# Optimization experiments

Measured on AMD Instinct MI355X. Metric: run time of the kernel, lower is better.

## Reference

```python
import jax, jax.numpy as jnp
import numpy as np

MAXDISP = 21  # default maxDisp from __init__


def _make_kernel():
    # convweights[i,0,:,0:2] = 1/6 ; convweights[i,0,:,i+2] = -1/3 ; bias[i] = i+1
    w = np.zeros((MAXDISP, 1, 3, MAXDISP + 2), dtype=np.float32)
    for i in range(MAXDISP):
        w[i, 0, :, 0:2] = 1.0 / 6.0
        w[i, 0, :, i + 2] = -1.0 / 3.0
    b = np.arange(1, MAXDISP + 1, dtype=np.float32)
    return jnp.asarray(w), jnp.asarray(b)


def _compute_mask(disp, w, b):
    # ReplicationPad2d((left=0, right=maxDisp+1, top=1, bottom=1))
    pad = jnp.pad(disp, ((0, 0), (0, 0), (1, 1), (0, MAXDISP + 1)), mode='edge')
    # conv2d, VALID: output spatial size == input spatial size
    out = jax.lax.conv_general_dilated(
        pad, w, window_strides=(1, 1), padding='VALID',
        dimension_numbers=('NCHW', 'OIHW', 'NCHW'))
    out = jnp.abs(out + b[None, :, None, None])          # [B, maxDisp, H, W]
    mask = jnp.min(out, axis=1, keepdims=True)           # channel-min -> [B,1,H,W]
    return jnp.clip(mask, 0.0, 1.0)


def _forward(dispmap, bsline):
    w, b = _make_kernel()
    maskl = _compute_mask(dispmap, w, b)
    # 'r' direction: flip along width, compute, flip back
    maskr = jnp.flip(_compute_mask(jnp.flip(dispmap, axis=3), w, b), axis=3)
    bs = bsline[:, None, None, None]
    zero = jnp.zeros_like(dispmap)
    # bsline < 0 -> left mask; bsline > 0 -> right mask; else zeros
    return jnp.where(bs < 0, maskl, jnp.where(bs > 0, maskr, zero))


def setup_inputs() -> dict:
    key = jax.random.key(0)
    k1, k2 = jax.random.split(key)
    # disparity-like values in [0, 1)
    dispmap = jax.random.uniform(k1, (8, 1, 384, 1280), dtype=jnp.float32)
    bsline = jax.random.normal(k2, (8,), dtype=jnp.float32)
    return {"dispmap": dispmap, "bsline": bsline}


def reference(dispmap, bsline):
    return _forward(dispmap, bsline)
```

## Files before the change

### kernel.cpp

```cpp
#include <hip/hip_runtime.h>

#define W 1280
#define H 384
#define ND 21

__global__ __launch_bounds__(256) void occl_kernel(const float* __restrict__ disp,
                                                   const float* __restrict__ bsl,
                                                   float* __restrict__ out) {
    const int row   = blockIdx.x % H;
    const int batch = blockIdx.x / H;
    const float bs  = bsl[batch];
    float* __restrict__ orow = out + (size_t)(batch * H + row) * W;

    if (bs == 0.0f) {
        for (int c = threadIdx.x; c < W; c += 256) orow[c] = 0.0f;
        return;
    }
    const int dir = (bs < 0.0f) ? 1 : -1;

    __shared__ float Cbuf[W + 48];
    float* Cs = Cbuf + 24;

    const float* __restrict__ dbase = disp + (size_t)batch * H * W;
    const float* __restrict__ r0 = dbase + (size_t)max(row - 1, 0) * W;
    const float* __restrict__ r1 = dbase + (size_t)row * W;
    const float* __restrict__ r2 = dbase + (size_t)min(row + 1, H - 1) * W;

    for (int c = threadIdx.x; c < W; c += 256) {
        Cs[c] = r0[c] + r1[c] + r2[c];
    }
    const int t = threadIdx.x;
    if (t < 22) {
        float cl = r0[0] + r1[0] + r2[0];
        Cs[-1 - t] = cl;
    } else if (t >= 64 && t < 86) {
        float cr = r0[W - 1] + r1[W - 1] + r2[W - 1];
        Cs[W + (t - 64)] = cr;
    }
    __syncthreads();

    for (int c = threadIdx.x; c < W; c += 256) {
        const float base = (1.0f / 6.0f) * (Cs[c] + Cs[c + dir]);
        int idx = c + 2 * dir;
        float m = 1e30f;
        #pragma unroll
        for (int i = 0; i < ND; i++) {
            float v = fabsf(base - (1.0f / 3.0f) * Cs[idx] + (float)(i + 1));
            m = fminf(m, v);
            idx += dir;
        }
        orow[c] = fminf(m, 1.0f);
    }
}

extern "C" void kernel_launch(void* const* d_in, const int* in_sizes, int n_in,
                              void* d_out, int out_size, void* d_ws, size_t ws_size,
                              hipStream_t stream) {
    const float* disp = (const float*)d_in[0];
    const float* bsl  = (const float*)d_in[1];
    float* out        = (float*)d_out;
    const int n_batch = in_sizes[1];

    dim3 grid(n_batch * H);
    occl_kernel<<<grid, 256, 0, stream>>>(disp, bsl, out);
}
```

Measured before the change: 78.03 us.

## Compute four columns per thread with float4 loads and register window reuse

Each thread now handles four adjacent columns. It loads its row sums with float4 accesses and pulls a 28-float window from shared memory into registers, so all four outputs reuse the same window. The shift direction is made a template parameter, which turns the indexing into compile-time constants. The block size becomes 320 so one block covers the whole row, and block IDs are remapped with an 8-way swizzle across the grid. In exchange the kernel uses more registers per thread and relies on the row width being exactly 1280.

```diff
diff --git a/kernel.cpp b/kernel.cpp
--- a/kernel.cpp
+++ b/kernel.cpp
@@ -1,22 +1,58 @@
 #include <hip/hip_runtime.h>
 
-#define W 1280
-#define H 384
+#define W  1280
+#define H  384
 #define ND 21
+#define BT 320
 
-__global__ __launch_bounds__(256) void occl_kernel(const float* __restrict__ disp,
-                                                   const float* __restrict__ bsl,
-                                                   float* __restrict__ out) {
-    const int row   = blockIdx.x % H;
-    const int batch = blockIdx.x / H;
-    const float bs  = bsl[batch];
+
+template <int DIR>
+__device__ __forceinline__ void compute4(const float* __restrict__ Cs,
+                                         float* __restrict__ orow, int t) {
+    float V[28];
+    const float4* p = (const float4*)(Cs + ((DIR > 0) ? 4 * t : 4 * t - 24));
+    #pragma unroll
+    for (int m = 0; m < 7; m++) {
+        float4 f = p[m];
+        V[4 * m + 0] = f.x; V[4 * m + 1] = f.y;
+        V[4 * m + 2] = f.z; V[4 * m + 3] = f.w;
+    }
+    float4 o;
+    float* op = &o.x;
+    #pragma unroll
+    for (int j = 0; j < 4; j++) {
+        float c0 = (DIR > 0) ? V[j]     : V[24 + j];
+        float c1 = (DIR > 0) ? V[j + 1] : V[23 + j];
+        float base = (c0 + c1) * (1.0f / 6.0f);
+        float m = 1e30f;
+        #pragma unroll
+        for (int i = 0; i < ND; i++) {
+            float ck = (DIR > 0) ? V[j + 2 + i] : V[22 + j - i];
+            float v = fabsf(base + (float)(i + 1) - ck * (1.0f / 3.0f));
+            m = fminf(m, v);
+        }
+        op[j] = fminf(m, 1.0f);
+    }
+    ((float4*)orow)[t] = o;
+}
+
+__global__ __launch_bounds__(BT) void occl_kernel(const float* __restrict__ disp,
+                                                  const float* __restrict__ bsl,
+                                                  float* __restrict__ out) {
+    int g = blockIdx.x;
+    int nb = gridDim.x;
+    int id = (nb & 7) ? g : ((g & 7) * (nb >> 3) + (g >> 3));
+    const int row = id % H;
+    const int batch = id / H;
+    const float bs = bsl[batch];
     float* __restrict__ orow = out + (size_t)(batch * H + row) * W;
+    const int t = threadIdx.x;
 
     if (bs == 0.0f) {
-        for (int c = threadIdx.x; c < W; c += 256) orow[c] = 0.0f;
+        float4 z = {0.0f, 0.0f, 0.0f, 0.0f};
+        ((float4*)orow)[t] = z;
         return;
     }
-    const int dir = (bs < 0.0f) ? 1 : -1;
 
     __shared__ float Cbuf[W + 48];
     float* Cs = Cbuf + 24;
@@ -26,31 +62,25 @@
     const float* __restrict__ r1 = dbase + (size_t)row * W;
     const float* __restrict__ r2 = dbase + (size_t)min(row + 1, H - 1) * W;
 
-    for (int c = threadIdx.x; c < W; c += 256) {
-        Cs[c] = r0[c] + r1[c] + r2[c];
-    }
-    const int t = threadIdx.x;
-    if (t < 22) {
-        float cl = r0[0] + r1[0] + r2[0];
-        Cs[-1 - t] = cl;
-    } else if (t >= 64 && t < 86) {
-        float cr = r0[W - 1] + r1[W - 1] + r2[W - 1];
-        Cs[W + (t - 64)] = cr;
+    float4 a = ((const float4*)r0)[t];
+    float4 b = ((const float4*)r1)[t];
+    float4 c = ((const float4*)r2)[t];
+    float4 s;
+    s.x = a.x + b.x + c.x;
+    s.y = a.y + b.y + c.y;
+    s.z = a.z + b.z + c.z;
+    s.w = a.w + b.w + c.w;
+    ((float4*)Cs)[t] = s;
+
+    if (t < 24) {
+        Cs[t - 24] = r0[0] + r1[0] + r2[0];
+    } else if (t >= 32 && t < 56) {
+        Cs[W + (t - 32)] = r0[W - 1] + r1[W - 1] + r2[W - 1];
     }
     __syncthreads();
 
-    for (int c = threadIdx.x; c < W; c += 256) {
-        const float base = (1.0f / 6.0f) * (Cs[c] + Cs[c + dir]);
-        int idx = c + 2 * dir;
-        float m = 1e30f;
-        #pragma unroll
-        for (int i = 0; i < ND; i++) {
-            float v = fabsf(base - (1.0f / 3.0f) * Cs[idx] + (float)(i + 1));
-            m = fminf(m, v);
-            idx += dir;
-        }
-        orow[c] = fminf(m, 1.0f);
-    }
+    if (bs < 0.0f) compute4<1>(Cs, orow, t);
+    else           compute4<-1>(Cs, orow, t);
 }
 
 extern "C" void kernel_launch(void* const* d_in, const int* in_sizes, int n_in,
@@ -61,6 +91,5 @@
     float* out        = (float*)d_out;
     const int n_batch = in_sizes[1];
 
-    dim3 grid(n_batch * H);
-    occl_kernel<<<grid, 256, 0, stream>>>(disp, bsl, out);
+    occl_kernel<<<dim3(n_batch * H), BT, 0, stream>>>(disp, bsl, out);
 }
```

Result: faster. 75.37 us (-3.4%).
